# Kernel tuning notes

Hardware: AMD Instinct MI355X
Metric: run time of the kernel (lower is better)

## Reference

```python
import jax, jax.numpy as jnp
import numpy as np


def setup_inputs() -> dict:
    key = jax.random.key(0)
    ks = jax.random.split(key, 6)
    b, t, s, qu, vu, d = 8, 64, 512, 512, 512, 512
    return {
        "query": jax.random.normal(ks[0], (b, t, qu), jnp.float32),
        "value": jax.random.normal(ks[1], (b, s, vu), jnp.float32),
        "mask": jax.random.randint(ks[2], (b, s), 0, 2).astype(bool),
        "W1_w": jax.random.normal(ks[3], (qu, d), jnp.float32) * (1.0 / np.sqrt(qu)),
        "W1_b": jnp.zeros((d,), jnp.float32),
        "W2_w": jax.random.normal(ks[4], (vu, d), jnp.float32) * (1.0 / np.sqrt(vu)),
        "W2_b": jnp.zeros((d,), jnp.float32),
        "scale": jax.random.normal(ks[5], (d,), jnp.float32) * 0.05,
    }


def reference(query, value, mask, W1_w, W1_b, W2_w, W2_b, scale):
    # Dense projections
    q = jnp.einsum('btq,qd->btd', query, W1_w) + W1_b   # [b,t,d]
    k = jnp.einsum('bsv,vd->bsd', value, W2_w) + W2_b   # [b,s,d]
    # Additive (Bahdanau) score with learned scale vector (Keras use_scale=True)
    # scores[b,t,s] = sum_d scale[d] * tanh(q[b,t,d] + k[b,s,d])
    scores = jnp.einsum('btsd,d->bts', jnp.tanh(q[:, :, None, :] + k[:, None, :, :]), scale)
    # Mask over source positions (value mask); query mask is all-ones (no-op)
    scores = jnp.where(mask[:, None, :], scores, jnp.float32(-1e9))
    attention_weights = jax.nn.softmax(scores, axis=-1)   # [b,t,s]
    context_vector = jnp.einsum('bts,bsv->btv', attention_weights, value)  # [b,t,vu]
    return context_vector, attention_weights
```

## Files before the change

kernel.cpp:

```cpp
#include <hip/hip_runtime.h>
#include <hip/hip_bf16.h>

#define B_  8
#define T_  64
#define S_  512
#define D_  512

#define QN (512 * 512)
#define KN (4096 * 512)

#define TLOG2E 2.8853900817779268f
#define LOG2E  1.4426950408889634f

typedef __attribute__((ext_vector_type(8))) short bf16x8;
typedef __attribute__((ext_vector_type(4))) float f32x4;

__device__ __forceinline__ unsigned int pk2(float a, float b) {
    float2 f; f.x = a; f.y = b;
    __hip_bfloat162 h = __float22bfloat162_rn(f);
    return *(unsigned int*)&h;
}
#define BF2X(U) __uint_as_float((U) << 16)
#define BF2Y(U) __uint_as_float((U) & 0xffff0000u)

__global__ __launch_bounds__(256) void mfma_gemm(
    const float* __restrict__ query, const float* __restrict__ value,
    const float* __restrict__ W1, const float* __restrict__ W2,
    const float* __restrict__ b1, const float* __restrict__ b2,
    float* __restrict__ qproj, unsigned short* __restrict__ kTb)
{
    __shared__ __align__(16) unsigned short Ab[2][64][72];
    __shared__ __align__(16) unsigned short Bs[2][64][72];

    const int x = blockIdx.x;
    const float *A, *W;
    int tm, tn;
    bool isq;
    if (x < 512) {
        tm = (x & 7) * 8 + ((x >> 3) & 7);
        tn = x >> 6;
        A = value; W = W2; isq = false;
    } else {
        int r = x - 512;
        tm = r >> 3; tn = r & 7;
        A = query; W = W1; isq = true;
    }

    const int tid  = threadIdx.x;
    const int lane = tid & 63;
    const int wid  = tid >> 6;
    const int wm = (wid & 1) * 32, wn = (wid >> 1) * 32;
    const int fm = lane & 15, fq = lane >> 4;

    f32x4 acc00 = {0.f, 0.f, 0.f, 0.f};
    f32x4 acc01 = acc00, acc10 = acc00, acc11 = acc00;

    const int ar = tid >> 2;
    const int kc = (tid & 3) * 16;
    const float* Ag = A + (size_t)(tm * 64 + ar) * 512 + kc;
    const int c0 = (tid & 15) * 4;
    const int kp = (tid >> 4) * 2;
    const float* Wg = W + (size_t)kp * 512 + tn * 64 + c0;

    float4 av0, av1, av2, av3;
    float4 wv0, wv1, wv2, wv3;

#define LOADT(KOFF) do {                                                      \
        av0 = *(const float4*)(Ag + (KOFF));                                  \
        av1 = *(const float4*)(Ag + (KOFF) + 4);                              \
        av2 = *(const float4*)(Ag + (KOFF) + 8);                              \
        av3 = *(const float4*)(Ag + (KOFF) + 12);                             \
        wv0 = *(const float4*)(Wg + (size_t)(KOFF) * 512);                    \
        wv1 = *(const float4*)(Wg + (size_t)(KOFF) * 512 + 512);              \
        wv2 = *(const float4*)(Wg + (size_t)((KOFF) + 32) * 512);             \
        wv3 = *(const float4*)(Wg + (size_t)((KOFF) + 32) * 512 + 512);       \
    } while (0)

#define STAGE(BUF) do {                                                       \
        uint4 p0, p1;                                                         \
        p0.x = pk2(av0.x, av0.y); p0.y = pk2(av0.z, av0.w);                   \
        p0.z = pk2(av1.x, av1.y); p0.w = pk2(av1.z, av1.w);                   \
        p1.x = pk2(av2.x, av2.y); p1.y = pk2(av2.z, av2.w);                   \
        p1.z = pk2(av3.x, av3.y); p1.w = pk2(av3.z, av3.w);                   \
        *(uint4*)&Ab[BUF][ar][kc]     = p0;                                   \
        *(uint4*)&Ab[BUF][ar][kc + 8] = p1;                                   \
        *(unsigned int*)&Bs[BUF][c0 + 0][kp]      = pk2(wv0.x, wv1.x);        \
        *(unsigned int*)&Bs[BUF][c0 + 1][kp]      = pk2(wv0.y, wv1.y);        \
        *(unsigned int*)&Bs[BUF][c0 + 2][kp]      = pk2(wv0.z, wv1.z);        \
        *(unsigned int*)&Bs[BUF][c0 + 3][kp]      = pk2(wv0.w, wv1.w);        \
        *(unsigned int*)&Bs[BUF][c0 + 0][kp + 32] = pk2(wv2.x, wv3.x);        \
        *(unsigned int*)&Bs[BUF][c0 + 1][kp + 32] = pk2(wv2.y, wv3.y);        \
        *(unsigned int*)&Bs[BUF][c0 + 2][kp + 32] = pk2(wv2.z, wv3.z);        \
        *(unsigned int*)&Bs[BUF][c0 + 3][kp + 32] = pk2(wv2.w, wv3.w);        \
    } while (0)

    LOADT(0);
    STAGE(0);
    LOADT(64);
    __syncthreads();

    for (int i = 0; i < 8; ++i) {
        const int cur = i & 1, nxt = cur ^ 1;
        bf16x8 a0, a1, b0, b1v;
#pragma unroll
        for (int kk = 0; kk < 64; kk += 32) {
            a0  = *(const bf16x8*)&Ab[cur][wm + fm][kk + fq * 8];
            a1  = *(const bf16x8*)&Ab[cur][wm + 16 + fm][kk + fq * 8];
            b0  = *(const bf16x8*)&Bs[cur][wn + fm][kk + fq * 8];
            b1v = *(const bf16x8*)&Bs[cur][wn + 16 + fm][kk + fq * 8];
            acc00 = __builtin_amdgcn_mfma_f32_16x16x32_bf16(a0, b0,  acc00, 0, 0, 0);
            acc01 = __builtin_amdgcn_mfma_f32_16x16x32_bf16(a0, b1v, acc01, 0, 0, 0);
            acc10 = __builtin_amdgcn_mfma_f32_16x16x32_bf16(a1, b0,  acc10, 0, 0, 0);
            acc11 = __builtin_amdgcn_mfma_f32_16x16x32_bf16(a1, b1v, acc11, 0, 0, 0);
        }
        if (i < 7) {
            STAGE(nxt);
            const int kn = ((i + 2) & 7) * 64;
            LOADT(kn);
        }
        __syncthreads();
    }
#undef STAGE
#undef LOADT

    const int n0 = tn * 64 + wn + fm;
    const int n1 = n0 + 16;
    const int m0 = tm * 64 + wm + fq * 4;
    if (isq) {
        float bias0 = b1[n0] + b2[n0];
        float bias1 = b1[n1] + b2[n1];
#pragma unroll
        for (int r = 0; r < 4; ++r) {
            qproj[(size_t)(m0 + r) * 512 + n0]      = (acc00[r] + bias0) * TLOG2E;
            qproj[(size_t)(m0 + r) * 512 + n1]      = (acc01[r] + bias1) * TLOG2E;
            qproj[(size_t)(m0 + 16 + r) * 512 + n0] = (acc10[r] + bias0) * TLOG2E;
            qproj[(size_t)(m0 + 16 + r) * 512 + n1] = (acc11[r] + bias1) * TLOG2E;
        }
    } else {
        const int bb = m0 >> 9;
        const int sl = m0 & 511;
        unsigned short* kb = kTb + (size_t)(bb * 512) * 512;
        uint2 o;
        o.x = pk2(acc00[0] * TLOG2E, acc00[1] * TLOG2E);
        o.y = pk2(acc00[2] * TLOG2E, acc00[3] * TLOG2E);
        *(uint2*)(kb + (size_t)n0 * 512 + sl) = o;
        o.x = pk2(acc10[0] * TLOG2E, acc10[1] * TLOG2E);
        o.y = pk2(acc10[2] * TLOG2E, acc10[3] * TLOG2E);
        *(uint2*)(kb + (size_t)n0 * 512 + sl + 16) = o;
        o.x = pk2(acc01[0] * TLOG2E, acc01[1] * TLOG2E);
        o.y = pk2(acc01[2] * TLOG2E, acc01[3] * TLOG2E);
        *(uint2*)(kb + (size_t)n1 * 512 + sl) = o;
        o.x = pk2(acc11[0] * TLOG2E, acc11[1] * TLOG2E);
        o.y = pk2(acc11[2] * TLOG2E, acc11[3] * TLOG2E);
        *(uint2*)(kb + (size_t)n1 * 512 + sl + 16) = o;
    }
}

__global__ __launch_bounds__(1024) void fused_attn(
    const float* __restrict__ qproj, const unsigned short* __restrict__ kTb,
    const int*   __restrict__ mask,  const float* __restrict__ scale,
    const float* __restrict__ value,
    float* __restrict__ ctx, float* __restrict__ attn)
{
    const int blk = blockIdx.x;
    const int b  = blk & 7;
    const int tp = blk >> 3;
    const size_t row0 = (size_t)(b * T_ + tp * 2);

    __shared__ __align__(16) float q0A[512];
    __shared__ __align__(16) float dA[512];
    __shared__ __align__(16) float cA[512];
    __shared__ __align__(16) float4 pex[4][256];
    __shared__ __align__(16) float2 wp2[512];
    __shared__ __align__(16) float4 part[2][8][128];
    __shared__ float2 red2[16];

    const int tid  = threadIdx.x;
    const int lane = tid & 63;
    const int wid  = tid >> 6;

    if (tid < 512) {
        float q0v = qproj[row0 * D_ + tid];
        float q1v = qproj[(row0 + 1) * D_ + tid];
        q0A[tid] = q0v;
        dA[tid]  = __builtin_amdgcn_exp2f(q1v - q0v);
        cA[tid]  = scale[tid];
    }
    __syncthreads();

    const int sp  = tid & 255;
    const int dq  = tid >> 8;
    const int dlo = dq * 128;
    const unsigned short* kb = kTb + ((size_t)(b * 512 + dlo)) * 512 + sp * 2;

    float p00 = 0.f, p10 = 0.f, p01 = 0.f, p11 = 0.f;

    unsigned int nf0 = *(const unsigned int*)(kb);
    unsigned int nf1 = *(const unsigned int*)(kb + 512);
    unsigned int nf2 = *(const unsigned int*)(kb + 1024);
    unsigned int nf3 = *(const unsigned int*)(kb + 1536);

#define SC2(KU, QV, DV, CV) do {                                              \
        float e0 = __builtin_amdgcn_exp2f((QV) + BF2X(KU));                   \
        float ra = __builtin_amdgcn_rcpf(e0 + 1.0f);                          \
        float rb = __builtin_amdgcn_rcpf(fmaf(e0, (DV), 1.0f));               \
        p00 = fmaf((CV), ra, p00); p10 = fmaf((CV), rb, p10);                 \
        float e1 = __builtin_amdgcn_exp2f((QV) + BF2Y(KU));                   \
        float rc = __builtin_amdgcn_rcpf(e1 + 1.0f);                          \
        float rd = __builtin_amdgcn_rcpf(fmaf(e1, (DV), 1.0f));               \
        p01 = fmaf((CV), rc, p01); p11 = fmaf((CV), rd, p11);                 \
    } while (0)

    for (int g = 0; g < 32; ++g) {
        unsigned int kf0 = nf0, kf1 = nf1, kf2 = nf2, kf3 = nf3;
        const unsigned short* nb = kb + (size_t)(((g + 1) & 31) * 4) * 512;
        nf0 = *(const unsigned int*)(nb);
        nf1 = *(const unsigned int*)(nb + 512);
        nf2 = *(const unsigned int*)(nb + 1024);
        nf3 = *(const unsigned int*)(nb + 1536);
        const int d0 = dlo + g * 4;
        float4 q4 = *(const float4*)&q0A[d0];
        float4 dl = *(const float4*)&dA[d0];
        float4 c4 = *(const float4*)&cA[d0];
        SC2(kf0, q4.x, dl.x, c4.x);
        SC2(kf1, q4.y, dl.y, c4.y);
        SC2(kf2, q4.z, dl.z, c4.z);
        SC2(kf3, q4.w, dl.w, c4.w);
    }
#undef SC2

    {
        float4 pq; pq.x = p00; pq.y = p10; pq.z = p01; pq.w = p11;
        pex[dq][sp] = pq;
    }
    __syncthreads();

    float x0 = 0.f, x1 = 0.f;
    if (tid < 512) {
        const int s = tid;
        const int s2 = s >> 1;
        const bool odd = (s & 1) != 0;
        float4 r0 = pex[0][s2], r1 = pex[1][s2];
        float4 r2 = pex[2][s2], r3 = pex[3][s2];
        float pt0 = odd ? ((r0.z + r1.z) + (r2.z + r3.z))
                        : ((r0.x + r1.x) + (r2.x + r3.x));
        float pt1 = odd ? ((r0.w + r1.w) + (r2.w + r3.w))
                        : ((r0.y + r1.y) + (r2.y + r3.y));
        const int m = mask[b * S_ + s];
        x0 = m ? (-2.0f * pt0) : -1e9f;
        x1 = m ? (-2.0f * pt1) : -1e9f;
        float2 mx; mx.x = x0; mx.y = x1;
#pragma unroll
        for (int off = 32; off >= 1; off >>= 1) {
            mx.x = fmaxf(mx.x, __shfl_xor(mx.x, off));
            mx.y = fmaxf(mx.y, __shfl_xor(mx.y, off));
        }
        if (lane == 0) red2[wid] = mx;
    }
    __syncthreads();

    float e0 = 0.f, e1 = 0.f;
    if (tid < 512) {
        float2 M = red2[0];
#pragma unroll
        for (int i = 1; i < 8; ++i) {
            M.x = fmaxf(M.x, red2[i].x);
            M.y = fmaxf(M.y, red2[i].y);
        }
        e0 = __builtin_amdgcn_exp2f((x0 - M.x) * LOG2E);
        e1 = __builtin_amdgcn_exp2f((x1 - M.y) * LOG2E);
        float2 sm; sm.x = e0; sm.y = e1;
#pragma unroll
        for (int off = 32; off >= 1; off >>= 1) {
            sm.x += __shfl_xor(sm.x, off);
            sm.y += __shfl_xor(sm.y, off);
        }
        if (lane == 0) red2[8 + wid] = sm;
    }
    __syncthreads();

    if (tid < 512) {
        const int s = tid;
        float2 SS = red2[8];
#pragma unroll
        for (int i = 9; i < 16; ++i) {
            SS.x += red2[i].x;
            SS.y += red2[i].y;
        }
        const float w0 = e0 * __builtin_amdgcn_rcpf(SS.x);
        const float w1 = e1 * __builtin_amdgcn_rcpf(SS.y);
        float2 wpair; wpair.x = w0; wpair.y = w1;
        wp2[s] = wpair;
        attn[row0 * S_ + s]       = w0;
        attn[(row0 + 1) * S_ + s] = w1;
    }
    __syncthreads();

    const int g  = tid >> 7;
    const int v4 = tid & 127;
    const float* vb = value + ((size_t)(b * S_) + g * 64) * D_ + v4 * 4;
    float4 a0; a0.x = 0.f; a0.y = 0.f; a0.z = 0.f; a0.w = 0.f;
    float4 a1 = a0;
#pragma unroll 4
    for (int i = 0; i < 64; ++i) {
        float4 vv = *(const float4*)(vb + (size_t)i * D_);
        float2 w = wp2[g * 64 + i];
        a0.x = fmaf(w.x, vv.x, a0.x); a0.y = fmaf(w.x, vv.y, a0.y);
        a0.z = fmaf(w.x, vv.z, a0.z); a0.w = fmaf(w.x, vv.w, a0.w);
        a1.x = fmaf(w.y, vv.x, a1.x); a1.y = fmaf(w.y, vv.y, a1.y);
        a1.z = fmaf(w.y, vv.z, a1.z); a1.w = fmaf(w.y, vv.w, a1.w);
    }
    part[0][g][v4] = a0;
    part[1][g][v4] = a1;
    __syncthreads();
    if (tid < 256) {
        const int t = tid >> 7, v = tid & 127;
        float4 o; o.x = 0.f; o.y = 0.f; o.z = 0.f; o.w = 0.f;
#pragma unroll
        for (int gg = 0; gg < 8; ++gg) {
            float4 p = part[t][gg][v];
            o.x += p.x; o.y += p.y; o.z += p.z; o.w += p.w;
        }
        *(float4*)(ctx + (row0 + t) * D_ + v * 4) = o;
    }
}

extern "C" void kernel_launch(void* const* d_in, const int* in_sizes, int n_in,
                              void* d_out, int out_size, void* d_ws, size_t ws_size,
                              hipStream_t stream) {
    const float* query = (const float*)d_in[0];
    const float* value = (const float*)d_in[1];
    const int*   mask  = (const int*)  d_in[2];
    const float* W1w   = (const float*)d_in[3];
    const float* W1b   = (const float*)d_in[4];
    const float* W2w   = (const float*)d_in[5];
    const float* W2b   = (const float*)d_in[6];
    const float* scale = (const float*)d_in[7];

    float* ctx  = (float*)d_out;
    float* attn = (float*)d_out + (size_t)B_ * T_ * D_;

    float* qproj = (float*)d_ws;
    unsigned short* kTb = (unsigned short*)(qproj + (size_t)QN);

    mfma_gemm<<<576, 256, 0, stream>>>(query, value, W1w, W2w, W1b, W2b,
                                       qproj, kTb);
    fused_attn<<<256, 1024, 0, stream>>>(qproj, kTb, mask, scale, value,
                                         ctx, attn);
}
```

Baseline: 126.1 us.

## Split context matmul into separate tiled kernel to reuse value across query rows

Moves the attention-weights × value product out of the fused attention kernel into a new ctx_gemm kernel. Each block handles 16 query rows and 64 value columns and stages value strips in shared memory. This cuts how often each value element is re-read, which was once per pair of query rows before. In exchange it adds a kernel launch and a round trip of the attention weights through global memory.

```diff
diff --git a/kernel.cpp b/kernel.cpp
--- a/kernel.cpp
+++ b/kernel.cpp
@@ -159,8 +159,7 @@
 __global__ __launch_bounds__(1024) void fused_attn(
     const float* __restrict__ qproj, const unsigned short* __restrict__ kTb,
     const int*   __restrict__ mask,  const float* __restrict__ scale,
-    const float* __restrict__ value,
-    float* __restrict__ ctx, float* __restrict__ attn)
+    float* __restrict__ attn)
 {
     const int blk = blockIdx.x;
     const int b  = blk & 7;
@@ -171,8 +170,6 @@
     __shared__ __align__(16) float dA[512];
     __shared__ __align__(16) float cA[512];
     __shared__ __align__(16) float4 pex[4][256];
-    __shared__ __align__(16) float2 wp2[512];
-    __shared__ __align__(16) float4 part[2][8][128];
     __shared__ float2 red2[16];
 
     const int tid  = threadIdx.x;
@@ -289,40 +286,70 @@
         }
         const float w0 = e0 * __builtin_amdgcn_rcpf(SS.x);
         const float w1 = e1 * __builtin_amdgcn_rcpf(SS.y);
-        float2 wpair; wpair.x = w0; wpair.y = w1;
-        wp2[s] = wpair;
         attn[row0 * S_ + s]       = w0;
         attn[(row0 + 1) * S_ + s] = w1;
     }
-    __syncthreads();
-
-    const int g  = tid >> 7;
-    const int v4 = tid & 127;
-    const float* vb = value + ((size_t)(b * S_) + g * 64) * D_ + v4 * 4;
-    float4 a0; a0.x = 0.f; a0.y = 0.f; a0.z = 0.f; a0.w = 0.f;
-    float4 a1 = a0;
+}
+
+__global__ __launch_bounds__(256) void ctx_gemm(
+    const float* __restrict__ attn, const float* __restrict__ value,
+    float* __restrict__ ctx)
+{
+    const int blk = blockIdx.x;
+    const int b  = blk & 7;
+    const int r  = blk >> 3;
+    const int tt = r & 3;
+    const int vc = r >> 2;
+
+    __shared__ __align__(16) float wA[16][516];
+    __shared__ __align__(16) float vS[64][64];
+
+    const int tid = threadIdx.x;
+
+    const float* ab = attn + (size_t)(b * T_ + tt * 16) * S_;
+#pragma unroll
+    for (int i = 0; i < 8; ++i) {
+        const int f   = i * 256 + tid;
+        const int row = f >> 7, c4 = f & 127;
+        *(float4*)&wA[row][c4 * 4] = *(const float4*)(ab + (size_t)row * S_ + c4 * 4);
+    }
+
+    const int t  = tid >> 4;
+    const int v4 = tid & 15;
+    const float* vb = value + (size_t)(b * S_) * D_ + vc * 64;
+
+    float4 acc; acc.x = 0.f; acc.y = 0.f; acc.z = 0.f; acc.w = 0.f;
+
+    for (int strip = 0; strip < 8; ++strip) {
+        __syncthreads();
+#pragma unroll
+        for (int j = 0; j < 4; ++j) {
+            const int f  = j * 256 + tid;
+            const int sr = f >> 4, c4 = f & 15;
+            *(float4*)&vS[sr][c4 * 4] =
+                *(const float4*)(vb + (size_t)(strip * 64 + sr) * D_ + c4 * 4);
+        }
+        __syncthreads();
+        const float* wrow = &wA[t][strip * 64];
 #pragma unroll 4
-    for (int i = 0; i < 64; ++i) {
-        float4 vv = *(const float4*)(vb + (size_t)i * D_);
-        float2 w = wp2[g * 64 + i];
-        a0.x = fmaf(w.x, vv.x, a0.x); a0.y = fmaf(w.x, vv.y, a0.y);
-        a0.z = fmaf(w.x, vv.z, a0.z); a0.w = fmaf(w.x, vv.w, a0.w);
-        a1.x = fmaf(w.y, vv.x, a1.x); a1.y = fmaf(w.y, vv.y, a1.y);
-        a1.z = fmaf(w.y, vv.z, a1.z); a1.w = fmaf(w.y, vv.w, a1.w);
-    }
-    part[0][g][v4] = a0;
-    part[1][g][v4] = a1;
-    __syncthreads();
-    if (tid < 256) {
-        const int t = tid >> 7, v = tid & 127;
-        float4 o; o.x = 0.f; o.y = 0.f; o.z = 0.f; o.w = 0.f;
-#pragma unroll
-        for (int gg = 0; gg < 8; ++gg) {
-            float4 p = part[t][gg][v];
-            o.x += p.x; o.y += p.y; o.z += p.z; o.w += p.w;
-        }
-        *(float4*)(ctx + (row0 + t) * D_ + v * 4) = o;
-    }
+        for (int s = 0; s < 64; s += 4) {
+            float4 w4 = *(const float4*)(wrow + s);
+            float4 va = *(const float4*)&vS[s + 0][v4 * 4];
+            acc.x = fmaf(w4.x, va.x, acc.x); acc.y = fmaf(w4.x, va.y, acc.y);
+            acc.z = fmaf(w4.x, va.z, acc.z); acc.w = fmaf(w4.x, va.w, acc.w);
+            float4 vbv = *(const float4*)&vS[s + 1][v4 * 4];
+            acc.x = fmaf(w4.y, vbv.x, acc.x); acc.y = fmaf(w4.y, vbv.y, acc.y);
+            acc.z = fmaf(w4.y, vbv.z, acc.z); acc.w = fmaf(w4.y, vbv.w, acc.w);
+            float4 vcv = *(const float4*)&vS[s + 2][v4 * 4];
+            acc.x = fmaf(w4.z, vcv.x, acc.x); acc.y = fmaf(w4.z, vcv.y, acc.y);
+            acc.z = fmaf(w4.z, vcv.z, acc.z); acc.w = fmaf(w4.z, vcv.w, acc.w);
+            float4 vdv = *(const float4*)&vS[s + 3][v4 * 4];
+            acc.x = fmaf(w4.w, vdv.x, acc.x); acc.y = fmaf(w4.w, vdv.y, acc.y);
+            acc.z = fmaf(w4.w, vdv.z, acc.z); acc.w = fmaf(w4.w, vdv.w, acc.w);
+        }
+    }
+
+    *(float4*)(ctx + (size_t)(b * T_ + tt * 16 + t) * D_ + vc * 64 + v4 * 4) = acc;
 }
 
 extern "C" void kernel_launch(void* const* d_in, const int* in_sizes, int n_in,
@@ -345,6 +372,6 @@
 
     mfma_gemm<<<576, 256, 0, stream>>>(query, value, W1w, W2w, W1b, W2b,
                                        qproj, kTb);
-    fused_attn<<<256, 1024, 0, stream>>>(qproj, kTb, mask, scale, value,
-                                         ctx, attn);
-}
+    fused_attn<<<256, 1024, 0, stream>>>(qproj, kTb, mask, scale, attn);
+    ctx_gemm<<<256, 256, 0, stream>>>(attn, value, ctx);
+}
```

Measured after the change: 130.9 us. 1.04x slower.
